# Kernel optimization log

Hardware: AMD Instinct MI355X
Metric: run time of the kernel (lower is better)

The kernel has to match this reference:

```python
import jax, jax.numpy as jnp
import numpy as np

D_MODEL = 1024
H = 16
D_K = D_MODEL // H
D_FF = 4096
EPS = 1e-6
NEG = -1e9


def layernorm(x, alpha, bias):
    # custom LN: unbiased std (ddof=1), scalar alpha/bias, divide by (std+eps)
    mean = jnp.mean(x, axis=-1, keepdims=True)
    n = x.shape[-1]
    var = jnp.sum((x - mean) ** 2, axis=-1, keepdims=True) / (n - 1)
    std = jnp.sqrt(var)
    return alpha * (x - mean) / (std + EPS) + bias


def setup_inputs() -> dict:
    key = jax.random.key(0)
    ks = jax.random.split(key, 16)
    B, S = 2, 2048
    s = 1.0 / np.sqrt(D_MODEL)
    inp = {
        "x": jax.random.normal(ks[0], (B, S, D_MODEL), jnp.float32),
        "src_mask": jnp.ones((B, 1, S), jnp.int32),
        "wq": jax.random.normal(ks[1], (D_MODEL, D_MODEL), jnp.float32) * s,
        "bq": jnp.zeros((D_MODEL,), jnp.float32),
        "wk": jax.random.normal(ks[2], (D_MODEL, D_MODEL), jnp.float32) * s,
        "bk": jnp.zeros((D_MODEL,), jnp.float32),
        "wv": jax.random.normal(ks[3], (D_MODEL, D_MODEL), jnp.float32) * s,
        "bv": jnp.zeros((D_MODEL,), jnp.float32),
        "wo": jax.random.normal(ks[4], (D_MODEL, D_MODEL), jnp.float32) * s,
        "bo": jnp.zeros((D_MODEL,), jnp.float32),
        "w1": jax.random.normal(ks[5], (D_MODEL, D_FF), jnp.float32) * s,
        "b1": jnp.zeros((D_FF,), jnp.float32),
        "w2": jax.random.normal(ks[6], (D_FF, D_MODEL), jnp.float32) * (1.0 / np.sqrt(D_FF)),
        "b2": jnp.zeros((D_MODEL,), jnp.float32),
        "ln1_a": jnp.ones((1,), jnp.float32),
        "ln1_b": jnp.zeros((1,), jnp.float32),
        "ln2_a": jnp.ones((1,), jnp.float32),
        "ln2_b": jnp.zeros((1,), jnp.float32),
    }
    return inp


def reference(x, src_mask, wq, bq, wk, bk, wv, bv, wo, bo,
              w1, b1, w2, b2, ln1_a, ln1_b, ln2_a, ln2_b):
    B, S, _ = x.shape
    # --- residual 1: pre-norm self attention ---
    xn = layernorm(x, ln1_a, ln1_b)
    q = (xn @ wq + bq).reshape(B, S, H, D_K)
    k = (xn @ wk + bk).reshape(B, S, H, D_K)
    v = (xn @ wv + bv).reshape(B, S, H, D_K)
    # scores [B, H, S, S]
    scores = jnp.einsum("bqhd,bkhd->bhqk", q, k) / jnp.sqrt(jnp.float32(D_K))
    m = src_mask[:, None, :, :]  # [B,1,1,S]
    scores = jnp.where(m == 0, NEG, scores)
    attn = jax.nn.softmax(scores, axis=-1)
    ctx = jnp.einsum("bhqk,bkhd->bqhd", attn, v).reshape(B, S, D_MODEL)
    attn_out = ctx @ wo + bo
    x = x + attn_out
    # --- residual 2: pre-norm FFN ---
    xn = layernorm(x, ln2_a, ln2_b)
    ff = jax.nn.relu(xn @ w1 + b1) @ w2 + b2
    return x + ff
```

## Files before the change

### kernel.cpp

```cpp
#include <hip/hip_runtime.h>
#include <hip/hip_bf16.h>

typedef __attribute__((ext_vector_type(8))) short short8;
typedef __attribute__((ext_vector_type(4))) float f32x4;
typedef __attribute__((ext_vector_type(4))) unsigned int u32x4;
using u16 = unsigned short;
typedef unsigned int u32;

__device__ __forceinline__ u16 f2bf(float f) {
    u32 u = __builtin_bit_cast(u32, f);
    u32 r = u + 0x7FFFu + ((u >> 16) & 1u);
    return (u16)(r >> 16);
}

__device__ __forceinline__ float exp2fast(float x) {
    return __builtin_amdgcn_exp2f(x);
}

__device__ __forceinline__ u32 cvtpk(float lo, float hi) {
    u32 r;
    asm("v_cvt_pk_bf16_f32 %0, %1, %2" : "=v"(r) : "v"(lo), "v"(hi));
    return r;
}

__device__ __forceinline__ void async_load16(const void* g, void* l) {
    __builtin_amdgcn_global_load_lds(
        (const __attribute__((address_space(1))) void*)g,
        (__attribute__((address_space(3))) void*)l, 16, 0, 0);
}

__global__ __launch_bounds__(256) void convt_kernel(const float* __restrict__ w,
                                                    u16* __restrict__ wt, int K, int N) {
    __shared__ float tile[32][33];
    int bn = blockIdx.x * 32, bk = blockIdx.y * 32;
    int tx = threadIdx.x & 31, ty = threadIdx.x >> 5;
#pragma unroll
    for (int i = 0; i < 4; i++)
        tile[ty + i * 8][tx] = w[(size_t)(bk + ty + i * 8) * N + bn + tx];
    __syncthreads();
#pragma unroll
    for (int i = 0; i < 4; i++)
        wt[(size_t)(bn + ty + i * 8) * K + bk + tx] = f2bf(tile[tx][ty + i * 8]);
}

__global__ __launch_bounds__(256) void convt4_kernel(const float* __restrict__ wa,
                                                     const float* __restrict__ wb,
                                                     const float* __restrict__ wc,
                                                     const float* __restrict__ wd,
                                                     u16* __restrict__ da,
                                                     u16* __restrict__ db,
                                                     u16* __restrict__ dc,
                                                     u16* __restrict__ dd) {
    __shared__ float tile[32][33];
    int z = blockIdx.z;
    const float* w = (z == 0) ? wa : (z == 1) ? wb : (z == 2) ? wc : wd;
    u16* wt = (z == 0) ? da : (z == 1) ? db : (z == 2) ? dc : dd;
    int bn = blockIdx.x * 32, bk = blockIdx.y * 32;
    int tx = threadIdx.x & 31, ty = threadIdx.x >> 5;
#pragma unroll
    for (int i = 0; i < 4; i++)
        tile[ty + i * 8][tx] = w[(size_t)(bk + ty + i * 8) * 1024 + bn + tx];
    __syncthreads();
#pragma unroll
    for (int i = 0; i < 4; i++)
        wt[(size_t)(bn + ty + i * 8) * 1024 + bk + tx] = f2bf(tile[tx][ty + i * 8]);
}

__global__ __launch_bounds__(256) void vtrans_kernel(const u16* __restrict__ qkv,
                                                     u16* __restrict__ vT) {
    __shared__ u16 tile[32][33];
    int bs = blockIdx.x * 32;
    int bc = blockIdx.y * 32;
    int b  = blockIdx.z;
    int tx = threadIdx.x & 31, ty = threadIdx.x >> 5;
#pragma unroll
    for (int i = 0; i < 4; i++)
        tile[ty + i * 8][tx] = qkv[(size_t)(b * 2048 + bs + ty + i * 8) * 3072 + 2048 + bc + tx];
    __syncthreads();
#pragma unroll
    for (int i = 0; i < 4; i++)
        vT[(size_t)(b * 1024 + bc + ty + i * 8) * 2048 + bs + tx] = tile[tx][ty + i * 8];
}

__global__ __launch_bounds__(256) void ln_kernel(const float* __restrict__ x,
                                                 const float* __restrict__ ga,
                                                 const float* __restrict__ gb,
                                                 u16* __restrict__ out) {
    int row = blockIdx.x;
    const float4* xr = (const float4*)(x + (size_t)row * 1024);
    float4 v = xr[threadIdx.x];
    float s  = v.x + v.y + v.z + v.w;
    float s2 = v.x * v.x + v.y * v.y + v.z * v.z + v.w * v.w;
#pragma unroll
    for (int off = 32; off; off >>= 1) {
        s  += __shfl_down(s, off);
        s2 += __shfl_down(s2, off);
    }
    __shared__ float rs[4], rs2[4];
    int wid = threadIdx.x >> 6, lane = threadIdx.x & 63;
    if (lane == 0) { rs[wid] = s; rs2[wid] = s2; }
    __syncthreads();
    float S  = rs[0] + rs[1] + rs[2] + rs[3];
    float S2 = rs2[0] + rs2[1] + rs2[2] + rs2[3];
    float mean = S * (1.0f / 1024.0f);
    float var  = fmaxf((S2 - 1024.0f * mean * mean) * (1.0f / 1023.0f), 0.0f);
    float scale = ga[0] / (sqrtf(var) + 1e-6f);
    float shift = gb[0] - mean * scale;
    u16 h0 = f2bf(v.x * scale + shift);
    u16 h1 = f2bf(v.y * scale + shift);
    u16 h2 = f2bf(v.z * scale + shift);
    u16 h3 = f2bf(v.w * scale + shift);
    uint2 pv;
    pv.x = (u32)h0 | ((u32)h1 << 16);
    pv.y = (u32)h2 | ((u32)h3 << 16);
    *(uint2*)(out + (size_t)row * 1024 + threadIdx.x * 4) = pv;
}

__global__ __launch_bounds__(256) void bias3_kernel(const float* __restrict__ a,
                                                    const float* __restrict__ b,
                                                    const float* __restrict__ c,
                                                    float* __restrict__ d) {
    int i = blockIdx.x * 256 + threadIdx.x;
    float v = (i < 1024) ? a[i] : ((i < 2048) ? b[i - 1024] : c[i - 2048]);
    d[i] = v;
}

__global__ __launch_bounds__(256) void addbias_kernel(float* __restrict__ dst,
                                                      const float* __restrict__ p,
                                                      const float* __restrict__ bias,
                                                      const float* __restrict__ resid) {
    int i4 = blockIdx.x * 256 + threadIdx.x;
    float4 d  = ((const float4*)dst)[i4];
    float4 pp = ((const float4*)p)[i4];
    float4 rr = ((const float4*)resid)[i4];
    float4 bb = *(const float4*)(bias + ((i4 * 4) & 1023));
    d.x += pp.x + bb.x + rr.x;
    d.y += pp.y + bb.y + rr.y;
    d.z += pp.z + bb.z + rr.z;
    d.w += pp.w + bb.w + rr.w;
    ((float4*)dst)[i4] = d;
}

template <int MODE, int RELU, int RESID>
__global__ __launch_bounds__(256) void gemm_bt(const u16* __restrict__ A,
                                               const u16* __restrict__ Bt,
                                               const float* __restrict__ bias,
                                               void* __restrict__ C0,
                                               void* __restrict__ C1,
                                               const float* __restrict__ resid,
                                               int M, int N, int K, int kLen) {
    __shared__ u16 As[8192];
    __shared__ u16 Bs[8192];
    int tid = threadIdx.x, lane = tid & 63, wid = tid >> 6;
    int l15 = lane & 15, l4 = lane >> 4;
    int rowA0 = blockIdx.x * 128;
    int rowB0 = blockIdx.y * 128;
    int kOff = blockIdx.z * kLen;
    void* Cout = blockIdx.z ? C1 : C0;
    int waveM = wid >> 1, waveN = wid & 1;

    int fl = tid * 8;
    int r0 = fl >> 5, c0 = fl & 31;
    const u16* gA0 = A + (size_t)(rowA0 + r0) * K + c0 + kOff;
    const u16* gA1 = A + (size_t)(rowA0 + 64 + r0) * K + c0 + kOff;
    const u16* gB0 = Bt + (size_t)(rowB0 + r0) * K + c0 + kOff;
    const u16* gB1 = Bt + (size_t)(rowB0 + 64 + r0) * K + c0 + kOff;

    f32x4 acc[4][4] = {};
    const int nIter = kLen >> 5;

    async_load16(gA0, As + wid * 512);
    async_load16(gA1, As + 2048 + wid * 512);
    async_load16(gB0, Bs + wid * 512);
    async_load16(gB1, Bs + 2048 + wid * 512);

    int cur = 0, kb = 32;
    for (int it = 0; it < nIter; ++it) {
        asm volatile("s_waitcnt vmcnt(0)" ::: "memory");
        __builtin_amdgcn_s_barrier();
        if (it + 1 < nIter) {
            u16* a = As + (cur ^ 1) * 4096;
            u16* bb = Bs + (cur ^ 1) * 4096;
            async_load16(gA0 + kb, a + wid * 512);
            async_load16(gA1 + kb, a + 2048 + wid * 512);
            async_load16(gB0 + kb, bb + wid * 512);
            async_load16(gB1 + kb, bb + 2048 + wid * 512);
        }
        __builtin_amdgcn_sched_barrier(0);

        const u16* a = As + cur * 4096;
        const u16* bb = Bs + cur * 4096;
        short8 af[4], bf[4];
#pragma unroll
        for (int m = 0; m < 4; m++)
            af[m] = *(const short8*)&a[(waveM * 64 + m * 16 + l15) * 32 + l4 * 8];
#pragma unroll
        for (int n = 0; n < 4; n++)
            bf[n] = *(const short8*)&bb[(waveN * 64 + n * 16 + l15) * 32 + l4 * 8];
#pragma unroll
        for (int m = 0; m < 4; m++)
#pragma unroll
            for (int n = 0; n < 4; n++)
                acc[m][n] = __builtin_amdgcn_mfma_f32_16x16x32_bf16(af[m], bf[n], acc[m][n], 0, 0, 0);

        __builtin_amdgcn_s_barrier();
        cur ^= 1;
        kb += 32;
    }

#pragma unroll
    for (int m = 0; m < 4; m++) {
        int row = rowA0 + waveM * 64 + m * 16 + l4 * 4;
#pragma unroll
        for (int n = 0; n < 4; n++) {
            int col = rowB0 + waveN * 64 + n * 16 + l15;
            float bc = (MODE == 2) ? 0.0f : bias[col];
#pragma unroll
            for (int j = 0; j < 4; j++) {
                float v = acc[m][n][j] + bc;
                if (RELU) v = fmaxf(v, 0.0f);
                if (RESID) v += resid[(size_t)(row + j) * N + col];
                if (MODE == 1)
                    ((u16*)Cout)[(size_t)(row + j) * N + col] = f2bf(v);
                else
                    ((float*)Cout)[(size_t)(row + j) * N + col] = v;
            }
        }
    }
}

__global__ __launch_bounds__(256) void attn_kernel(const u16* __restrict__ qkv,
                                                   const u16* __restrict__ vT,
                                                   const int* __restrict__ mask,
                                                   u16* __restrict__ ctx) {
    const int S = 2048;
    const float C = 0.180336880f;
    int qt = blockIdx.x;
    int bh = blockIdx.y;
    int b = bh >> 4, h = bh & 15;
    int tid = threadIdx.x;
    int wid = tid >> 6, lane = tid & 63;
    int l15 = lane & 15, l4 = lane >> 4;

    __shared__ u16 Ks[64][72];
    __shared__ u16 Vs[64][72];
    __shared__ u32 PT[4][16][38];
    __shared__ int mflag;

    if (tid == 0) mflag = 1;
    __syncthreads();
    {
        const int* mrow = mask + b * S;
        int ok = 1;
#pragma unroll
        for (int i = 0; i < 8; i++) ok &= (mrow[tid * 8 + i] != 0);
        if (!ok) mflag = 0;
    }

    int qrow0 = qt * 64 + wid * 16;
    const u16* qb = qkv + (size_t)(b * S + qrow0) * 3072 + h * 64;
    short8 qf0 = *(const short8*)(qb + (size_t)l15 * 3072 + l4 * 8);
    short8 qf1 = *(const short8*)(qb + (size_t)l15 * 3072 + 32 + l4 * 8);

    f32x4 o[4] = {};
    float m_i = -1e30f, lp = 0.0f;
    __syncthreads();
    const int allones = mflag;
    const int* mrow = mask + b * S;

    int srow = tid >> 3, c8 = (tid & 7) * 8;
    short8 kreg[2], vreg[2];
#pragma unroll
    for (int p = 0; p < 2; p++) {
        int r = p * 32 + srow;
        kreg[p] = *(const short8*)(qkv + (size_t)(b * S + r) * 3072 + 1024 + h * 64 + c8);
        vreg[p] = *(const short8*)(vT + (size_t)(bh * 64 + r) * 2048 + c8);
    }

    for (int kt = 0; kt < 32; ++kt) {
        __builtin_amdgcn_s_barrier();
#pragma unroll
        for (int p = 0; p < 2; p++) {
            int r = p * 32 + srow;
            *(short8*)&Ks[r][c8] = kreg[p];
            *(short8*)&Vs[r][c8] = vreg[p];
        }
        if (kt + 1 < 32) {
#pragma unroll
            for (int p = 0; p < 2; p++) {
                int r = p * 32 + srow;
                kreg[p] = *(const short8*)(qkv + (size_t)(b * S + (kt + 1) * 64 + r) * 3072 + 1024 + h * 64 + c8);
                vreg[p] = *(const short8*)(vT + (size_t)(bh * 64 + r) * 2048 + (kt + 1) * 64 + c8);
            }
        }
        asm volatile("s_waitcnt lgkmcnt(0)" ::: "memory");
        __builtin_amdgcn_s_barrier();

        float sc[4][4];
#pragma unroll
        for (int kc = 0; kc < 4; kc++) {
            short8 kf0 = *(const short8*)&Ks[kc * 16 + l15][l4 * 8];
            short8 kf1 = *(const short8*)&Ks[kc * 16 + l15][32 + l4 * 8];
            f32x4 a = {};
            a = __builtin_amdgcn_mfma_f32_16x16x32_bf16(kf0, qf0, a, 0, 0, 0);
            a = __builtin_amdgcn_mfma_f32_16x16x32_bf16(kf1, qf1, a, 0, 0, 0);
            if (allones) {
#pragma unroll
                for (int j = 0; j < 4; j++) sc[kc][j] = a[j];
            } else {
#pragma unroll
                for (int j = 0; j < 4; j++) {
                    int mk = mrow[kt * 64 + kc * 16 + l4 * 4 + j];
                    sc[kc][j] = mk ? a[j] : -1e9f;
                }
            }
        }

        float lm = sc[0][0];
#pragma unroll
        for (int kc = 0; kc < 4; kc++)
#pragma unroll
            for (int j = 0; j < 4; j++) lm = fmaxf(lm, sc[kc][j]);
        if (!__all(lm <= m_i + 64.0f)) {
            float t = lm;
            t = fmaxf(t, __shfl_xor(t, 16));
            t = fmaxf(t, __shfl_xor(t, 32));
            float newm = fmaxf(m_i, t);
            float r = exp2fast((m_i - newm) * C);
            lp *= r;
            float rr0 = __shfl(r, l4 * 4 + 0);
            float rr1 = __shfl(r, l4 * 4 + 1);
            float rr2 = __shfl(r, l4 * 4 + 2);
            float rr3 = __shfl(r, l4 * 4 + 3);
#pragma unroll
            for (int dc = 0; dc < 4; dc++) {
                o[dc][0] *= rr0; o[dc][1] *= rr1; o[dc][2] *= rr2; o[dc][3] *= rr3;
            }
            m_i = newm;
        }

        float nb = -m_i * C;
#pragma unroll
        for (int kc = 0; kc < 4; kc++) {
            float p0 = exp2fast(fmaf(sc[kc][0], C, nb));
            float p1 = exp2fast(fmaf(sc[kc][1], C, nb));
            float p2 = exp2fast(fmaf(sc[kc][2], C, nb));
            float p3 = exp2fast(fmaf(sc[kc][3], C, nb));
            lp += (p0 + p1) + (p2 + p3);
            uint2 w;
            w.x = cvtpk(p0, p1);
            w.y = cvtpk(p2, p3);
            *(uint2*)&PT[wid][l15][kc * 8 + l4 * 2] = w;
        }

        uint2 r01 = *(const uint2*)&PT[wid][l15][l4 * 4];
        uint2 r23 = *(const uint2*)&PT[wid][l15][l4 * 4 + 2];
        uint2 r45 = *(const uint2*)&PT[wid][l15][16 + l4 * 4];
        uint2 r67 = *(const uint2*)&PT[wid][l15][16 + l4 * 4 + 2];
        u32x4 w0 = {r01.x, r01.y, r23.x, r23.y};
        u32x4 w1 = {r45.x, r45.y, r67.x, r67.y};
        short8 pa0 = __builtin_bit_cast(short8, w0);
        short8 pa1 = __builtin_bit_cast(short8, w1);

#pragma unroll
        for (int dc = 0; dc < 4; dc++) {
            short8 vf0 = *(const short8*)&Vs[dc * 16 + l15][l4 * 8];
            short8 vf1 = *(const short8*)&Vs[dc * 16 + l15][32 + l4 * 8];
            o[dc] = __builtin_amdgcn_mfma_f32_16x16x32_bf16(pa0, vf0, o[dc], 0, 0, 0);
            o[dc] = __builtin_amdgcn_mfma_f32_16x16x32_bf16(pa1, vf1, o[dc], 0, 0, 0);
        }
    }

    float lt = lp;
    lt += __shfl_xor(lt, 16);
    lt += __shfl_xor(lt, 32);
    float inv = 1.0f / lt;
    float iv0 = __shfl(inv, l4 * 4 + 0);
    float iv1 = __shfl(inv, l4 * 4 + 1);
    float iv2 = __shfl(inv, l4 * 4 + 2);
    float iv3 = __shfl(inv, l4 * 4 + 3);
#pragma unroll
    for (int j = 0; j < 4; j++) {
        float ivj = (j == 0) ? iv0 : (j == 1) ? iv1 : (j == 2) ? iv2 : iv3;
        int row = qrow0 + l4 * 4 + j;
        size_t base = (size_t)(b * S + row) * 1024 + h * 64;
#pragma unroll
        for (int dc = 0; dc < 4; dc++)
            ctx[base + dc * 16 + l15] = f2bf(o[dc][j] * ivj);
    }
}

extern "C" void kernel_launch(void* const* d_in, const int* in_sizes, int n_in,
                              void* d_out, int out_size, void* d_ws, size_t ws_size,
                              hipStream_t stream) {
    const float* x    = (const float*)d_in[0];
    const int*   mask = (const int*)d_in[1];
    const float* wq   = (const float*)d_in[2];
    const float* bq   = (const float*)d_in[3];
    const float* wk   = (const float*)d_in[4];
    const float* bk   = (const float*)d_in[5];
    const float* wv   = (const float*)d_in[6];
    const float* bv   = (const float*)d_in[7];
    const float* wo   = (const float*)d_in[8];
    const float* bo   = (const float*)d_in[9];
    const float* w1   = (const float*)d_in[10];
    const float* b1   = (const float*)d_in[11];
    const float* w2   = (const float*)d_in[12];
    const float* b2   = (const float*)d_in[13];
    const float* ln1a = (const float*)d_in[14];
    const float* ln1b = (const float*)d_in[15];
    const float* ln2a = (const float*)d_in[16];
    const float* ln2b = (const float*)d_in[17];
    float* out = (float*)d_out;

    char* ws = (char*)d_ws;
    u16*   wqkvt = (u16*)(ws + 0);
    u16*   wot   = (u16*)(ws + 6291456);
    u16*   w1t   = (u16*)(ws + 8388608);
    u16*   w2t   = (u16*)(ws + 16777216);
    float* bqkv  = (float*)(ws + 25165824);
    char*  regA  = ws + 26214400;
    u16*   xn1   = (u16*)(regA + 0);
    u16*   vT    = (u16*)(regA + 0);
    u16*   qkv   = (u16*)(regA + 8388608);
    u16*   ctx   = (u16*)(regA + 33554432);
    float* p0wo  = (float*)(regA + 0);
    float* x1    = (float*)(ws + 68157440);
    u16*   xn2   = (u16*)(regA + 0);
    u16*   ff1   = (u16*)(regA + 8388608);
    float* p0f2  = (float*)(ws + 0);

    dim3 blk(256);

    convt4_kernel<<<dim3(32, 32, 4), blk, 0, stream>>>(
        wq, wk, wv, wo, wqkvt, wqkvt + 1024 * 1024, wqkvt + 2048 * 1024, wot);
    convt_kernel<<<dim3(128, 32), blk, 0, stream>>>(w1, w1t, 1024, 4096);
    convt_kernel<<<dim3(32, 128), blk, 0, stream>>>(w2, w2t, 4096, 1024);
    bias3_kernel<<<dim3(12), blk, 0, stream>>>(bq, bk, bv, bqkv);

    ln_kernel<<<dim3(4096), blk, 0, stream>>>(x, ln1a, ln1b, xn1);
    gemm_bt<1, 0, 0><<<dim3(32, 24, 1), blk, 0, stream>>>(xn1, wqkvt, bqkv, qkv, qkv, nullptr,
                                                          4096, 3072, 1024, 1024);
    vtrans_kernel<<<dim3(64, 32, 2), blk, 0, stream>>>(qkv, vT);
    attn_kernel<<<dim3(32, 32), blk, 0, stream>>>(qkv, vT, mask, ctx);
    gemm_bt<2, 0, 0><<<dim3(32, 8, 2), blk, 0, stream>>>(ctx, wot, nullptr, p0wo, x1, nullptr,
                                                         4096, 1024, 1024, 512);
    addbias_kernel<<<dim3(4096), blk, 0, stream>>>(x1, p0wo, bo, x);

    ln_kernel<<<dim3(4096), blk, 0, stream>>>(x1, ln2a, ln2b, xn2);
    gemm_bt<1, 1, 0><<<dim3(32, 32, 1), blk, 0, stream>>>(xn2, w1t, b1, ff1, ff1, nullptr,
                                                          4096, 4096, 1024, 1024);
    gemm_bt<2, 0, 0><<<dim3(32, 8, 2), blk, 0, stream>>>(ff1, w2t, nullptr, p0f2, out, nullptr,
                                                         4096, 1024, 4096, 2048);
    addbias_kernel<<<dim3(4096), blk, 0, stream>>>(out, p0f2, b2, x1);
}
```

Before: 277.0 us.

## Add 256x256-tile 512-thread GEMM for QKV/FFN1 and shuffle-based P repack in attention

Introduces a new GEMM kernel with 256x256 output tiles, 8 waves, double-buffered async global-to-LDS loads with XOR swizzle, bid swizzling and setprio around MFMA bursts, and uses it for the QKV projection and the first FFN GEMM. This is meant to raise arithmetic intensity and overlap loads with compute. Separately, the attention kernel replaces the LDS round-trip for repacking softmax probabilities into the MFMA A-operand layout with cross-lane shuffles. The larger tiles launch fewer blocks (192 and 256 workgroups), which may underfill the 256 CUs. They also use 128 KB of LDS per block.

```diff
diff --git a/kernel.cpp b/kernel.cpp
--- a/kernel.cpp
+++ b/kernel.cpp
@@ -27,6 +27,12 @@
     __builtin_amdgcn_global_load_lds(
         (const __attribute__((address_space(1))) void*)g,
         (__attribute__((address_space(3))) void*)l, 16, 0, 0);
+}
+
+__device__ __forceinline__ void wg_barrier() {
+    asm volatile("" ::: "memory");
+    __builtin_amdgcn_s_barrier();
+    asm volatile("" ::: "memory");
 }
 
 __global__ __launch_bounds__(256) void convt_kernel(const float* __restrict__ w,
@@ -141,6 +147,115 @@
     ((float4*)dst)[i4] = d;
 }
 
+template <int RELU>
+__global__ __launch_bounds__(512) void gemm256_bt(const u16* __restrict__ A,
+                                                  const u16* __restrict__ Bt,
+                                                  const float* __restrict__ bias,
+                                                  u16* __restrict__ C,
+                                                  int M, int N, int K, int tilesN) {
+    __shared__ u16 lds[2][2][16384];
+    const int tid = threadIdx.x;
+    const int lane = tid & 63, wid = tid >> 6;
+    const int l15 = lane & 15, l4 = lane >> 4;
+    const int wm = wid >> 2, wn = wid & 3;
+
+    int nwg = gridDim.x;
+    int bid = blockIdx.x;
+    int swz = (bid & 7) * (nwg >> 3) + (bid >> 3);
+    int ty = swz / tilesN, tx = swz % tilesN;
+
+    const u16* Ag = A + (size_t)(ty * 256) * K;
+    const u16* Bg = Bt + (size_t)(tx * 256) * K;
+
+    auto stage_half = [&](int slot, int ab, int half, const u16* G, int k0) {
+#pragma unroll
+        for (int j = 0; j < 2; j++) {
+            int off16 = half * 1024 + j * 512 + tid;
+            int r = off16 >> 3;
+            int gs = (off16 & 7) ^ (r & 7);
+            const u16* src = G + (size_t)r * K + k0 + gs * 8;
+            u16* dst = &lds[slot][ab][(size_t)(half * 1024 + j * 512 + (wid << 6)) * 8];
+            async_load16(src, dst);
+        }
+    };
+
+    f32x4 acc[8][4] = {};
+    const int nT = K >> 6;
+
+    stage_half(0, 0, 0, Ag, 0);
+    stage_half(0, 0, 1, Ag, 0);
+    stage_half(0, 1, 0, Bg, 0);
+    stage_half(0, 1, 1, Bg, 0);
+    __builtin_amdgcn_sched_barrier(0);
+
+    for (int t = 0; t < nT; ++t) {
+        const int cs = t & 1, ns = cs ^ 1;
+        const int k1 = (t + 1) << 6;
+        const bool pf = (t + 1 < nT);
+#pragma unroll
+        for (int ph = 0; ph < 4; ++ph) {
+            if (ph == 0 && pf) { stage_half(ns, 0, 0, Ag, k1); stage_half(ns, 0, 1, Ag, k1); }
+            if (ph == 1 && pf) { stage_half(ns, 1, 0, Bg, k1); stage_half(ns, 1, 1, Bg, k1); }
+            __builtin_amdgcn_sched_barrier(0);
+            if (ph == 0) {
+                if (pf) asm volatile("s_waitcnt vmcnt(4)" ::: "memory");
+                else    asm volatile("s_waitcnt vmcnt(0)" ::: "memory");
+            }
+            wg_barrier();
+
+            const int rh = ph >> 1, ch = ph & 1;
+            const u16* la = &lds[cs][0][0];
+            const u16* lb = &lds[cs][1][0];
+            short8 af[4][2], bf[2][2];
+#pragma unroll
+            for (int m2 = 0; m2 < 4; m2++) {
+                int ra = wm * 128 + rh * 64 + m2 * 16 + l15;
+#pragma unroll
+                for (int ks = 0; ks < 2; ks++) {
+                    int sl = (l4 + ks * 4) ^ (ra & 7);
+                    af[m2][ks] = *(const short8*)&la[ra * 64 + sl * 8];
+                }
+            }
+#pragma unroll
+            for (int n2 = 0; n2 < 2; n2++) {
+                int rb = wn * 64 + ch * 32 + n2 * 16 + l15;
+#pragma unroll
+                for (int ks = 0; ks < 2; ks++) {
+                    int sl = (l4 + ks * 4) ^ (rb & 7);
+                    bf[n2][ks] = *(const short8*)&lb[rb * 64 + sl * 8];
+                }
+            }
+            __builtin_amdgcn_s_setprio(1);
+#pragma unroll
+            for (int m2 = 0; m2 < 4; m2++)
+#pragma unroll
+                for (int n2 = 0; n2 < 2; n2++)
+#pragma unroll
+                    for (int ks = 0; ks < 2; ks++)
+                        acc[rh * 4 + m2][ch * 2 + n2] = __builtin_amdgcn_mfma_f32_16x16x32_bf16(
+                            af[m2][ks], bf[n2][ks], acc[rh * 4 + m2][ch * 2 + n2], 0, 0, 0);
+            __builtin_amdgcn_s_setprio(0);
+            wg_barrier();
+        }
+    }
+
+#pragma unroll
+    for (int mi = 0; mi < 8; mi++) {
+        int row0 = ty * 256 + wm * 128 + (mi >> 2) * 64 + (mi & 3) * 16 + l4 * 4;
+#pragma unroll
+        for (int ni = 0; ni < 4; ni++) {
+            int col = tx * 256 + wn * 64 + (ni >> 1) * 32 + (ni & 1) * 16 + l15;
+            float bc = bias[col];
+#pragma unroll
+            for (int jj = 0; jj < 4; jj++) {
+                float v = acc[mi][ni][jj] + bc;
+                if (RELU) v = fmaxf(v, 0.0f);
+                C[(size_t)(row0 + jj) * N + col] = f2bf(v);
+            }
+        }
+    }
+}
+
 template <int MODE, int RELU, int RESID>
 __global__ __launch_bounds__(256) void gemm_bt(const u16* __restrict__ A,
                                                const u16* __restrict__ Bt,
@@ -244,7 +359,6 @@
 
     __shared__ u16 Ks[64][72];
     __shared__ u16 Vs[64][72];
-    __shared__ u32 PT[4][16][38];
     __shared__ int mflag;
 
     if (tid == 0) mflag = 1;
@@ -340,6 +454,7 @@
         }
 
         float nb = -m_i * C;
+        u32 pk[4][2];
 #pragma unroll
         for (int kc = 0; kc < 4; kc++) {
             float p0 = exp2fast(fmaf(sc[kc][0], C, nb));
@@ -347,20 +462,26 @@
             float p2 = exp2fast(fmaf(sc[kc][2], C, nb));
             float p3 = exp2fast(fmaf(sc[kc][3], C, nb));
             lp += (p0 + p1) + (p2 + p3);
-            uint2 w;
-            w.x = cvtpk(p0, p1);
-            w.y = cvtpk(p2, p3);
-            *(uint2*)&PT[wid][l15][kc * 8 + l4 * 2] = w;
-        }
-
-        uint2 r01 = *(const uint2*)&PT[wid][l15][l4 * 4];
-        uint2 r23 = *(const uint2*)&PT[wid][l15][l4 * 4 + 2];
-        uint2 r45 = *(const uint2*)&PT[wid][l15][16 + l4 * 4];
-        uint2 r67 = *(const uint2*)&PT[wid][l15][16 + l4 * 4 + 2];
-        u32x4 w0 = {r01.x, r01.y, r23.x, r23.y};
-        u32x4 w1 = {r45.x, r45.y, r67.x, r67.y};
-        short8 pa0 = __builtin_bit_cast(short8, w0);
-        short8 pa1 = __builtin_bit_cast(short8, w1);
+            pk[kc][0] = cvtpk(p0, p1);
+            pk[kc][1] = cvtpk(p2, p3);
+        }
+
+        u32 w0[4], w1[4];
+#pragma unroll
+        for (int i = 0; i < 4; i++) {
+            int idx = l15 + (((2 * l4 + (i >> 1)) & 3) << 4);
+            int tt = i & 1;
+            u32 a0 = (u32)__shfl((int)pk[0][tt], idx);
+            u32 a1 = (u32)__shfl((int)pk[1][tt], idx);
+            u32 a2 = (u32)__shfl((int)pk[2][tt], idx);
+            u32 a3 = (u32)__shfl((int)pk[3][tt], idx);
+            w0[i] = (l4 < 2) ? a0 : a1;
+            w1[i] = (l4 < 2) ? a2 : a3;
+        }
+        u32x4 v0 = {w0[0], w0[1], w0[2], w0[3]};
+        u32x4 v1 = {w1[0], w1[1], w1[2], w1[3]};
+        short8 pa0 = __builtin_bit_cast(short8, v0);
+        short8 pa1 = __builtin_bit_cast(short8, v1);
 
 #pragma unroll
         for (int dc = 0; dc < 4; dc++) {
@@ -439,8 +560,7 @@
     bias3_kernel<<<dim3(12), blk, 0, stream>>>(bq, bk, bv, bqkv);
 
     ln_kernel<<<dim3(4096), blk, 0, stream>>>(x, ln1a, ln1b, xn1);
-    gemm_bt<1, 0, 0><<<dim3(32, 24, 1), blk, 0, stream>>>(xn1, wqkvt, bqkv, qkv, qkv, nullptr,
-                                                          4096, 3072, 1024, 1024);
+    gemm256_bt<0><<<dim3(192), dim3(512), 0, stream>>>(xn1, wqkvt, bqkv, qkv, 4096, 3072, 1024, 12);
     vtrans_kernel<<<dim3(64, 32, 2), blk, 0, stream>>>(qkv, vT);
     attn_kernel<<<dim3(32, 32), blk, 0, stream>>>(qkv, vT, mask, ctx);
     gemm_bt<2, 0, 0><<<dim3(32, 8, 2), blk, 0, stream>>>(ctx, wot, nullptr, p0wo, x1, nullptr,
@@ -448,8 +568,7 @@
     addbias_kernel<<<dim3(4096), blk, 0, stream>>>(x1, p0wo, bo, x);
 
     ln_kernel<<<dim3(4096), blk, 0, stream>>>(x1, ln2a, ln2b, xn2);
-    gemm_bt<1, 1, 0><<<dim3(32, 32, 1), blk, 0, stream>>>(xn2, w1t, b1, ff1, ff1, nullptr,
-                                                          4096, 4096, 1024, 1024);
+    gemm256_bt<1><<<dim3(256), dim3(512), 0, stream>>>(xn2, w1t, b1, ff1, 4096, 4096, 1024, 16);
     gemm_bt<2, 0, 0><<<dim3(32, 8, 2), blk, 0, stream>>>(ff1, w2t, nullptr, p0f2, out, nullptr,
                                                          4096, 1024, 4096, 2048);
     addbias_kernel<<<dim3(4096), blk, 0, stream>>>(out, p0f2, b2, x1);
```

Result: no change. 279.9 us (+1.0%).
